# Optimization experiments

Hardware: AMD Instinct MI355X
Metric: run time of the kernel (lower is better)

The kernel has to match this reference:

```python
import jax, jax.numpy as jnp
import numpy as np

HIDDEN = 1024

def setup_inputs() -> dict:
    key = jax.random.key(0)
    k1, k2, k3 = jax.random.split(key, 3)
    X = jax.random.normal(k1, (4, 2048, HIDDEN), dtype=jnp.float32)
    W = jax.random.normal(k2, (HIDDEN, 3 * HIDDEN), dtype=jnp.float32) * (1.0 / np.sqrt(HIDDEN))
    b = jax.random.normal(k3, (3 * HIDDEN,), dtype=jnp.float32) * 0.02
    return {"X": X, "W": W, "b": b}

def reference(X, W, b):
    D = X.shape[-1]
    # fused QKV projection: [B,S,3D]
    QKV = jnp.einsum('bsd,de->bse', X, W) + b
    Q, K, V = jnp.split(QKV, 3, axis=-1)
    # full attention scores [B,S,S]
    scores = jnp.einsum('bqd,bkd->bqk', Q, K) / jnp.sqrt(jnp.float32(D))
    attn = jax.nn.softmax(scores, axis=-1)
    out = jnp.einsum('bqk,bkd->bqd', attn, V)
    return out
```

## Files before the change

kernel.cpp:

```cpp
#include <hip/hip_runtime.h>

typedef unsigned short u16;
typedef unsigned int   u32;
typedef __attribute__((ext_vector_type(8))) short bf16x8;
typedef __attribute__((ext_vector_type(4))) float f32x4;
typedef __attribute__((ext_vector_type(4))) unsigned short us4;

__device__ __forceinline__ u16 f2bf(float f) {
    union { float f; u32 u; } v; v.f = f;
    u32 u = v.u;
    return (u16)((u + 0x7fffu + ((u >> 16) & 1u)) >> 16);
}

__device__ __forceinline__ void gload_lds16(const void* g, void* l) {
    __builtin_amdgcn_global_load_lds((const __attribute__((address_space(1))) u32*)g,
                                     (__attribute__((address_space(3))) u32*)l,
                                     16, 0, 0);
}

template<bool OUT_BF16, bool ADD_BIAS>
__global__ __launch_bounds__(256)
void gemm_bt(const u16* __restrict__ A, int lda, size_t strA,
             const u16* __restrict__ B, int ldb, size_t strB,
             void* __restrict__ Cv, int ldc, size_t strC,
             const float* __restrict__ bias, int K, float alpha)
{
    __shared__ __align__(16) u16 As[128 * 32];
    __shared__ __align__(16) u16 Bs[128 * 32];

    const int tid  = threadIdx.x;
    const int w    = tid >> 6;
    const int lane = tid & 63;
    const int wm   = w >> 1, wn = w & 1;
    const int m0   = blockIdx.y * 128, n0 = blockIdx.x * 128;
    const int fm   = lane & 15, fq = lane >> 4;

    A += (size_t)blockIdx.z * strA;
    B += (size_t)blockIdx.z * strB;

    f32x4 acc[4][4] = {};

    for (int k0 = 0; k0 < K; k0 += 32) {
#pragma unroll
        for (int h = 0; h < 2; ++h) {
            const int cb = h * 256 + w * 64;
            const int c  = cb + lane;
            gload_lds16(A + (size_t)(m0 + (c >> 2)) * lda + (k0 + (c & 3) * 8),
                        (char*)As + cb * 16);
            gload_lds16(B + (size_t)(n0 + (c >> 2)) * ldb + (k0 + (c & 3) * 8),
                        (char*)Bs + cb * 16);
        }
        __syncthreads();

        bf16x8 af[4], bv[4];
#pragma unroll
        for (int i = 0; i < 4; ++i)
            af[i] = *(const bf16x8*)(As + (wm * 64 + i * 16 + fm) * 32 + fq * 8);
#pragma unroll
        for (int j = 0; j < 4; ++j)
            bv[j] = *(const bf16x8*)(Bs + (wn * 64 + j * 16 + fm) * 32 + fq * 8);
#pragma unroll
        for (int i = 0; i < 4; ++i)
#pragma unroll
            for (int j = 0; j < 4; ++j)
                acc[i][j] = __builtin_amdgcn_mfma_f32_16x16x32_bf16(af[i], bv[j], acc[i][j], 0, 0, 0);
        __syncthreads();
    }

    float bval[4];
    if (ADD_BIAS) {
#pragma unroll
        for (int j = 0; j < 4; ++j) bval[j] = bias[n0 + wn * 64 + j * 16 + fm];
    }
#pragma unroll
    for (int i = 0; i < 4; ++i) {
        const int row = m0 + wm * 64 + i * 16 + fq * 4;
#pragma unroll
        for (int j = 0; j < 4; ++j) {
            const int col = n0 + wn * 64 + j * 16 + fm;
#pragma unroll
            for (int r = 0; r < 4; ++r) {
                float v = acc[i][j][r] * alpha;
                if (ADD_BIAS) v += bval[j];
                if (OUT_BF16)
                    ((u16*)Cv)[(size_t)blockIdx.z * strC + (size_t)(row + r) * ldc + col] = f2bf(v);
                else
                    ((float*)Cv)[(size_t)blockIdx.z * strC + (size_t)(row + r) * ldc + col] = v;
            }
        }
    }
}

__global__ __launch_bounds__(256)
void convert_x(const float* __restrict__ X, u16* __restrict__ Xb, int n4)
{
    int i = blockIdx.x * blockDim.x + threadIdx.x;
    if (i < n4) {
        float4 v = ((const float4*)X)[i];
        us4 o = { f2bf(v.x), f2bf(v.y), f2bf(v.z), f2bf(v.w) };
        ((us4*)Xb)[i] = o;
    }
}

__global__ __launch_bounds__(256)
void transpose_w(const float* __restrict__ W, u16* __restrict__ Wt)
{
    __shared__ u16 t[64][65];
    const int k0 = blockIdx.x * 64, n0 = blockIdx.y * 64;
    const int tx = threadIdx.x, ty = threadIdx.y;
#pragma unroll
    for (int i = 0; i < 64; i += 4)
        t[ty + i][tx] = f2bf(W[(size_t)(k0 + ty + i) * 3072 + n0 + tx]);
    __syncthreads();
#pragma unroll
    for (int i = 0; i < 64; i += 4)
        Wt[(size_t)(n0 + ty + i) * 1024 + k0 + tx] = t[tx][ty + i];
}

__global__ __launch_bounds__(256)
void transpose_v(const u16* __restrict__ QKV, u16* __restrict__ Vt)
{
    __shared__ u16 t[64][65];
    const int b  = blockIdx.z;
    const int d0 = blockIdx.x * 64, s0 = blockIdx.y * 64;
    const int tx = threadIdx.x, ty = threadIdx.y;
    const u16* src = QKV + (size_t)(b * 2048 + s0) * 3072 + 2048 + d0;
#pragma unroll
    for (int i = 0; i < 64; i += 4)
        t[ty + i][tx] = src[(size_t)(ty + i) * 3072 + tx];
    __syncthreads();
    u16* dst = Vt + (size_t)b * 1024 * 2048 + (size_t)d0 * 2048 + s0;
#pragma unroll
    for (int i = 0; i < 64; i += 4)
        dst[(size_t)(ty + i) * 2048 + tx] = t[tx][ty + i];
}

__global__ __launch_bounds__(256)
void softmax_rows(float* __restrict__ S)
{
    __shared__ float redm[4], reds[4];
    const size_t row = blockIdx.x;
    float* sr = S + row * 2048;
    const int t = threadIdx.x;

    float4 a = ((const float4*)sr)[t];
    float4 b = ((const float4*)sr)[t + 256];

    float mx = fmaxf(fmaxf(fmaxf(a.x, a.y), fmaxf(a.z, a.w)),
                     fmaxf(fmaxf(b.x, b.y), fmaxf(b.z, b.w)));
#pragma unroll
    for (int o = 32; o; o >>= 1) mx = fmaxf(mx, __shfl_xor(mx, o));
    if ((t & 63) == 0) redm[t >> 6] = mx;
    __syncthreads();
    mx = fmaxf(fmaxf(redm[0], redm[1]), fmaxf(redm[2], redm[3]));

    float e[8];
    e[0] = __expf(a.x - mx); e[1] = __expf(a.y - mx);
    e[2] = __expf(a.z - mx); e[3] = __expf(a.w - mx);
    e[4] = __expf(b.x - mx); e[5] = __expf(b.y - mx);
    e[6] = __expf(b.z - mx); e[7] = __expf(b.w - mx);
    float s = ((e[0] + e[1]) + (e[2] + e[3])) + ((e[4] + e[5]) + (e[6] + e[7]));
#pragma unroll
    for (int o = 32; o; o >>= 1) s += __shfl_xor(s, o);
    if ((t & 63) == 0) reds[t >> 6] = s;
    __syncthreads();
    s = reds[0] + reds[1] + reds[2] + reds[3];
    const float inv = 1.0f / s;

    u16* pr = (u16*)sr;
    us4 o1 = { f2bf(e[0] * inv), f2bf(e[1] * inv), f2bf(e[2] * inv), f2bf(e[3] * inv) };
    us4 o2 = { f2bf(e[4] * inv), f2bf(e[5] * inv), f2bf(e[6] * inv), f2bf(e[7] * inv) };
    ((us4*)pr)[t]       = o1;
    ((us4*)pr)[t + 256] = o2;
}

extern "C" void kernel_launch(void* const* d_in, const int* in_sizes, int n_in,
                              void* d_out, int out_size, void* d_ws, size_t ws_size,
                              hipStream_t stream)
{
    const float* X    = (const float*)d_in[0];
    const float* W    = (const float*)d_in[1];
    const float* bias = (const float*)d_in[2];
    float* out = (float*)d_out;
    char* ws = (char*)d_ws;

    u16*   QKV = (u16*)ws;
    u16*   Vt  = (u16*)(ws + 50331648);
    float* S   = (float*)(ws + 67108864);
    u16*   Xb  = (u16*)(ws + 67108864);
    u16*   Wt  = (u16*)(ws + 83886080);

    convert_x<<<8192, 256, 0, stream>>>(X, Xb, 8192 * 1024 / 4);
    transpose_w<<<dim3(16, 48), dim3(64, 4), 0, stream>>>(W, Wt);

    gemm_bt<true, true><<<dim3(24, 64, 1), 256, 0, stream>>>(
        Xb, 1024, 0, Wt, 1024, 0, QKV, 3072, 0, bias, 1024, 1.0f);

    transpose_v<<<dim3(16, 32, 4), dim3(64, 4), 0, stream>>>(QKV, Vt);

    gemm_bt<false, false><<<dim3(16, 16, 4), 256, 0, stream>>>(
        QKV,        3072, (size_t)2048 * 3072,
        QKV + 1024, 3072, (size_t)2048 * 3072,
        S,          2048, (size_t)2048 * 2048,
        nullptr, 1024, 0.03125f);

    softmax_rows<<<8192, 256, 0, stream>>>(S);

    gemm_bt<false, false><<<dim3(8, 16, 4), 256, 0, stream>>>(
        (const u16*)S, 4096, (size_t)2048 * 4096,
        Vt,            2048, (size_t)1024 * 2048,
        out,           1024, (size_t)2048 * 1024,
        nullptr, 2048, 1.0f);
}
```

Measured before the change: 310.7 us.

## Use 32x32 MFMA with swizzled LDS and store attention scores in bf16

The GEMM now uses 32x32x16 bf16 MFMA tiles with an XOR-style swizzled LDS layout, and precomputes global and LDS offsets outside the k-loop. The goal is fewer LDS bank conflicts and fewer fragment loads per MFMA. The score GEMM now writes bf16 instead of fp32, and softmax reads and writes bf16 in place. This halves traffic on the large score matrix at the cost of rounding the scores to bf16 before softmax.

New measurement: 287.9 us. 1.08x faster.

```diff
diff --git a/kernel.cpp b/kernel.cpp
--- a/kernel.cpp
+++ b/kernel.cpp
@@ -2,14 +2,20 @@
 
 typedef unsigned short u16;
 typedef unsigned int   u32;
-typedef __attribute__((ext_vector_type(8))) short bf16x8;
-typedef __attribute__((ext_vector_type(4))) float f32x4;
-typedef __attribute__((ext_vector_type(4))) unsigned short us4;
+typedef __attribute__((ext_vector_type(8)))  short bf16x8;
+typedef __attribute__((ext_vector_type(16))) float f32x16;
+typedef __attribute__((ext_vector_type(4)))  unsigned short us4;
 
 __device__ __forceinline__ u16 f2bf(float f) {
     union { float f; u32 u; } v; v.f = f;
     u32 u = v.u;
     return (u16)((u + 0x7fffu + ((u >> 16) & 1u)) >> 16);
+}
+__device__ __forceinline__ float bf2f_lo(u32 p) {
+    union { u32 u; float f; } t; t.u = p << 16; return t.f;
+}
+__device__ __forceinline__ float bf2f_hi(u32 p) {
+    union { u32 u; float f; } t; t.u = p & 0xffff0000u; return t.f;
 }
 
 __device__ __forceinline__ void gload_lds16(const void* g, void* l) {
@@ -33,59 +39,82 @@
     const int lane = tid & 63;
     const int wm   = w >> 1, wn = w & 1;
     const int m0   = blockIdx.y * 128, n0 = blockIdx.x * 128;
-    const int fm   = lane & 15, fq = lane >> 4;
+    const int l31  = lane & 31, lh = lane >> 5;
 
     A += (size_t)blockIdx.z * strA;
     B += (size_t)blockIdx.z * strB;
 
-    f32x4 acc[4][4] = {};
+    size_t goffA[2], goffB[2];
+#pragma unroll
+    for (int h = 0; h < 2; ++h) {
+        const int c = h * 256 + w * 64 + lane;
+        const int r = c >> 2;
+        const int q = ((c & 3) - (r >> 1)) & 3;
+        goffA[h] = (size_t)(m0 + r) * lda + q * 8;
+        goffB[h] = (size_t)(n0 + r) * ldb + q * 8;
+    }
+
+    int offA[2][2], offB[2][2];
+#pragma unroll
+    for (int i = 0; i < 2; ++i) {
+        const int ra = wm * 64 + i * 32 + l31;
+        const int rb = wn * 64 + i * 32 + l31;
+#pragma unroll
+        for (int ks = 0; ks < 2; ++ks) {
+            const int qq = ks * 2 + lh;
+            offA[i][ks] = (ra * 4 + ((qq + (ra >> 1)) & 3)) * 16;
+            offB[i][ks] = (rb * 4 + ((qq + (rb >> 1)) & 3)) * 16;
+        }
+    }
+
+    f32x16 acc[2][2] = {};
 
     for (int k0 = 0; k0 < K; k0 += 32) {
-#pragma unroll
-        for (int h = 0; h < 2; ++h) {
-            const int cb = h * 256 + w * 64;
-            const int c  = cb + lane;
-            gload_lds16(A + (size_t)(m0 + (c >> 2)) * lda + (k0 + (c & 3) * 8),
-                        (char*)As + cb * 16);
-            gload_lds16(B + (size_t)(n0 + (c >> 2)) * ldb + (k0 + (c & 3) * 8),
-                        (char*)Bs + cb * 16);
-        }
+        gload_lds16(A + goffA[0] + k0, (char*)As + (w * 64) * 16);
+        gload_lds16(A + goffA[1] + k0, (char*)As + (256 + w * 64) * 16);
+        gload_lds16(B + goffB[0] + k0, (char*)Bs + (w * 64) * 16);
+        gload_lds16(B + goffB[1] + k0, (char*)Bs + (256 + w * 64) * 16);
         __syncthreads();
 
-        bf16x8 af[4], bv[4];
-#pragma unroll
-        for (int i = 0; i < 4; ++i)
-            af[i] = *(const bf16x8*)(As + (wm * 64 + i * 16 + fm) * 32 + fq * 8);
-#pragma unroll
-        for (int j = 0; j < 4; ++j)
-            bv[j] = *(const bf16x8*)(Bs + (wn * 64 + j * 16 + fm) * 32 + fq * 8);
-#pragma unroll
-        for (int i = 0; i < 4; ++i)
-#pragma unroll
-            for (int j = 0; j < 4; ++j)
-                acc[i][j] = __builtin_amdgcn_mfma_f32_16x16x32_bf16(af[i], bv[j], acc[i][j], 0, 0, 0);
+        bf16x8 af[2][2], bfr[2][2];
+#pragma unroll
+        for (int i = 0; i < 2; ++i)
+#pragma unroll
+            for (int ks = 0; ks < 2; ++ks) {
+                af[i][ks]  = *(const bf16x8*)((const char*)As + offA[i][ks]);
+                bfr[i][ks] = *(const bf16x8*)((const char*)Bs + offB[i][ks]);
+            }
+#pragma unroll
+        for (int ks = 0; ks < 2; ++ks)
+#pragma unroll
+            for (int i = 0; i < 2; ++i)
+#pragma unroll
+                for (int j = 0; j < 2; ++j)
+                    acc[i][j] = __builtin_amdgcn_mfma_f32_32x32x16_bf16(
+                        af[i][ks], bfr[j][ks], acc[i][j], 0, 0, 0);
         __syncthreads();
     }
 
-    float bval[4];
+    float bval[2];
     if (ADD_BIAS) {
 #pragma unroll
-        for (int j = 0; j < 4; ++j) bval[j] = bias[n0 + wn * 64 + j * 16 + fm];
-    }
-#pragma unroll
-    for (int i = 0; i < 4; ++i) {
-        const int row = m0 + wm * 64 + i * 16 + fq * 4;
-#pragma unroll
-        for (int j = 0; j < 4; ++j) {
-            const int col = n0 + wn * 64 + j * 16 + fm;
-#pragma unroll
-            for (int r = 0; r < 4; ++r) {
+        for (int j = 0; j < 2; ++j) bval[j] = bias[n0 + wn * 64 + j * 32 + l31];
+    }
+#pragma unroll
+    for (int i = 0; i < 2; ++i) {
+        const int rowb = m0 + wm * 64 + i * 32 + 4 * lh;
+#pragma unroll
+        for (int j = 0; j < 2; ++j) {
+            const int col = n0 + wn * 64 + j * 32 + l31;
+#pragma unroll
+            for (int r = 0; r < 16; ++r) {
+                const int row = rowb + (r & 3) + 8 * (r >> 2);
                 float v = acc[i][j][r] * alpha;
                 if (ADD_BIAS) v += bval[j];
                 if (OUT_BF16)
-                    ((u16*)Cv)[(size_t)blockIdx.z * strC + (size_t)(row + r) * ldc + col] = f2bf(v);
+                    ((u16*)Cv)[(size_t)blockIdx.z * strC + (size_t)row * ldc + col] = f2bf(v);
                 else
-                    ((float*)Cv)[(size_t)blockIdx.z * strC + (size_t)(row + r) * ldc + col] = v;
+                    ((float*)Cv)[(size_t)blockIdx.z * strC + (size_t)row * ldc + col] = v;
             }
         }
     }
@@ -136,30 +165,30 @@
 }
 
 __global__ __launch_bounds__(256)
-void softmax_rows(float* __restrict__ S)
+void softmax_rows(u16* __restrict__ S)
 {
     __shared__ float redm[4], reds[4];
-    const size_t row = blockIdx.x;
-    float* sr = S + row * 2048;
+    u16* sr = S + (size_t)blockIdx.x * 2048;
     const int t = threadIdx.x;
 
-    float4 a = ((const float4*)sr)[t];
-    float4 b = ((const float4*)sr)[t + 256];
-
-    float mx = fmaxf(fmaxf(fmaxf(a.x, a.y), fmaxf(a.z, a.w)),
-                     fmaxf(fmaxf(b.x, b.y), fmaxf(b.z, b.w)));
+    uint4 raw = ((const uint4*)sr)[t];
+    float x[8];
+    x[0] = bf2f_lo(raw.x); x[1] = bf2f_hi(raw.x);
+    x[2] = bf2f_lo(raw.y); x[3] = bf2f_hi(raw.y);
+    x[4] = bf2f_lo(raw.z); x[5] = bf2f_hi(raw.z);
+    x[6] = bf2f_lo(raw.w); x[7] = bf2f_hi(raw.w);
+
+    float mx = fmaxf(fmaxf(fmaxf(x[0], x[1]), fmaxf(x[2], x[3])),
+                     fmaxf(fmaxf(x[4], x[5]), fmaxf(x[6], x[7])));
 #pragma unroll
     for (int o = 32; o; o >>= 1) mx = fmaxf(mx, __shfl_xor(mx, o));
     if ((t & 63) == 0) redm[t >> 6] = mx;
     __syncthreads();
     mx = fmaxf(fmaxf(redm[0], redm[1]), fmaxf(redm[2], redm[3]));
 
-    float e[8];
-    e[0] = __expf(a.x - mx); e[1] = __expf(a.y - mx);
-    e[2] = __expf(a.z - mx); e[3] = __expf(a.w - mx);
-    e[4] = __expf(b.x - mx); e[5] = __expf(b.y - mx);
-    e[6] = __expf(b.z - mx); e[7] = __expf(b.w - mx);
-    float s = ((e[0] + e[1]) + (e[2] + e[3])) + ((e[4] + e[5]) + (e[6] + e[7]));
+    float e[8], s = 0.f;
+#pragma unroll
+    for (int k = 0; k < 8; ++k) { e[k] = __expf(x[k] - mx); s += e[k]; }
 #pragma unroll
     for (int o = 32; o; o >>= 1) s += __shfl_xor(s, o);
     if ((t & 63) == 0) reds[t >> 6] = s;
@@ -167,11 +196,12 @@
     s = reds[0] + reds[1] + reds[2] + reds[3];
     const float inv = 1.0f / s;
 
-    u16* pr = (u16*)sr;
-    us4 o1 = { f2bf(e[0] * inv), f2bf(e[1] * inv), f2bf(e[2] * inv), f2bf(e[3] * inv) };
-    us4 o2 = { f2bf(e[4] * inv), f2bf(e[5] * inv), f2bf(e[6] * inv), f2bf(e[7] * inv) };
-    ((us4*)pr)[t]       = o1;
-    ((us4*)pr)[t + 256] = o2;
+    uint4 o4;
+    o4.x = (u32)f2bf(e[0] * inv) | ((u32)f2bf(e[1] * inv) << 16);
+    o4.y = (u32)f2bf(e[2] * inv) | ((u32)f2bf(e[3] * inv) << 16);
+    o4.z = (u32)f2bf(e[4] * inv) | ((u32)f2bf(e[5] * inv) << 16);
+    o4.w = (u32)f2bf(e[6] * inv) | ((u32)f2bf(e[7] * inv) << 16);
+    ((uint4*)sr)[t] = o4;
 }
 
 extern "C" void kernel_launch(void* const* d_in, const int* in_sizes, int n_in,
@@ -184,11 +214,11 @@
     float* out = (float*)d_out;
     char* ws = (char*)d_ws;
 
-    u16*   QKV = (u16*)ws;
-    u16*   Vt  = (u16*)(ws + 50331648);
-    float* S   = (float*)(ws + 67108864);
-    u16*   Xb  = (u16*)(ws + 67108864);
-    u16*   Wt  = (u16*)(ws + 83886080);
+    u16* QKV = (u16*)ws;
+    u16* Vt  = (u16*)(ws + 50331648);
+    u16* S   = (u16*)(ws + 67108864);
+    u16* Xb  = (u16*)(ws + 67108864);
+    u16* Wt  = (u16*)(ws + 83886080);
 
     convert_x<<<8192, 256, 0, stream>>>(X, Xb, 8192 * 1024 / 4);
     transpose_w<<<dim3(16, 48), dim3(64, 4), 0, stream>>>(W, Wt);
@@ -198,7 +228,7 @@
 
     transpose_v<<<dim3(16, 32, 4), dim3(64, 4), 0, stream>>>(QKV, Vt);
 
-    gemm_bt<false, false><<<dim3(16, 16, 4), 256, 0, stream>>>(
+    gemm_bt<true, false><<<dim3(16, 16, 4), 256, 0, stream>>>(
         QKV,        3072, (size_t)2048 * 3072,
         QKV + 1024, 3072, (size_t)2048 * 3072,
         S,          2048, (size_t)2048 * 2048,
@@ -207,8 +237,8 @@
     softmax_rows<<<8192, 256, 0, stream>>>(S);
 
     gemm_bt<false, false><<<dim3(8, 16, 4), 256, 0, stream>>>(
-        (const u16*)S, 4096, (size_t)2048 * 4096,
-        Vt,            2048, (size_t)1024 * 2048,
-        out,           1024, (size_t)2048 * 1024,
+        S,  2048, (size_t)2048 * 2048,
+        Vt, 2048, (size_t)1024 * 2048,
+        out, 1024, (size_t)2048 * 1024,
         nullptr, 2048, 1.0f);
 }
```
